# Optimization experiments

Measured on AMD Instinct MI355X. Metric: run time of the kernel, lower is better.

The kernel has to match this reference:

```python
import jax, jax.numpy as jnp
import numpy as np

B, H, I, E = 65536, 1024, 1024, 16

def setup_inputs() -> dict:
    key = jax.random.key(0)
    k1, k2, k3 = jax.random.split(key, 3)
    x = jax.random.normal(k1, (B, H), dtype=jnp.float32)
    Wg = jax.random.normal(k2, (E, H), dtype=jnp.float32) * 0.02   # gate weight [E, H]
    We = jax.random.normal(k3, (E, I, H), dtype=jnp.float32) * 0.02  # stacked expert weights [E, I, H]
    return {"x": x, "Wg": Wg, "We": We}

def reference(x, Wg, We):
    # gate scores and top-1 routing
    scores = x @ Wg.T                       # [B, E]
    expert_idx = jnp.argmax(scores, axis=-1)  # [B]
    onehot = jax.nn.one_hot(expert_idx, We.shape[0], dtype=x.dtype)  # [B, E]
    # each token goes through exactly one expert; sum of masked-input GEMMs
    out = jnp.zeros((x.shape[0], We.shape[1]), dtype=x.dtype)
    for e in range(We.shape[0]):  # fixed small expert count
        out = out + (x * onehot[:, e:e + 1]) @ We[e].T
    return out
```

## Files before the change

kernel.cpp:

```cpp
#include <hip/hip_runtime.h>
#include <hip/hip_bf16.h>

#define B_TOK 65536
#define HDIM  1024
#define EXP   16
#define IDIM  1024

typedef __attribute__((ext_vector_type(8))) short bf16x8_t;
typedef __attribute__((ext_vector_type(4))) float f32x4_t;


__device__ __forceinline__ unsigned short f2bf(float f) {
    unsigned int u = __float_as_uint(f);
    unsigned int r = (u + 0x7FFFu + ((u >> 16) & 1u)) >> 16;
    return (unsigned short)r;
}

__device__ __forceinline__ void async_load16(const void* g, void* l) {
    __builtin_amdgcn_global_load_lds(
        (const __attribute__((address_space(1))) unsigned int*)g,
        (__attribute__((address_space(3))) unsigned int*)l,
        16, 0, 0);
}

__global__ __launch_bounds__(256) void gate_kernel(
    const float* __restrict__ x, const float* __restrict__ Wg,
    unsigned short* __restrict__ xbf, int* __restrict__ eidx,
    int* __restrict__ cnts)
{
    __shared__ float wg[EXP * HDIM];
    const int tid = threadIdx.x;
    if (blockIdx.x == 0 && tid < EXP) cnts[tid] = 0;
    {
        const f32x4_t* s = (const f32x4_t*)Wg;
        f32x4_t* d = (f32x4_t*)wg;
        for (int i = tid; i < EXP * HDIM / 4; i += 256) d[i] = s[i];
    }
    __syncthreads();

    const int wid = tid >> 6, lane = tid & 63;
    const int gw = blockIdx.x * 4 + wid;

    for (int it = 0; it < 4; ++it) {
        const int t0 = gw * 16 + it * 4;
        f32x4_t xv[4][4];
        float acc[4][EXP];
        #pragma unroll
        for (int t = 0; t < 4; ++t) {
            const f32x4_t* row = (const f32x4_t*)(x + (size_t)(t0 + t) * HDIM);
            #pragma unroll
            for (int j = 0; j < 4; ++j)
                xv[t][j] = __builtin_nontemporal_load(row + j * 64 + lane);
        }
        #pragma unroll
        for (int t = 0; t < 4; ++t)
            #pragma unroll
            for (int e = 0; e < EXP; ++e) acc[t][e] = 0.f;

        #pragma unroll
        for (int j = 0; j < 4; ++j) {
            #pragma unroll
            for (int e = 0; e < EXP; ++e) {
                f32x4_t wv = *(const f32x4_t*)(wg + e * HDIM + j * 256 + lane * 4);
                #pragma unroll
                for (int t = 0; t < 4; ++t) {
                    acc[t][e] += xv[t][j][0] * wv[0] + xv[t][j][1] * wv[1]
                               + xv[t][j][2] * wv[2] + xv[t][j][3] * wv[3];
                }
            }
        }
        #pragma unroll
        for (int t = 0; t < 4; ++t) {
            unsigned short* orow = xbf + (size_t)(t0 + t) * HDIM;
            #pragma unroll
            for (int j = 0; j < 4; ++j) {
                ushort4 o;
                o.x = f2bf(xv[t][j][0]); o.y = f2bf(xv[t][j][1]);
                o.z = f2bf(xv[t][j][2]); o.w = f2bf(xv[t][j][3]);
                *(ushort4*)(orow + j * 256 + lane * 4) = o;
            }
        }
        #pragma unroll
        for (int t = 0; t < 4; ++t) {
            #pragma unroll
            for (int d = 32; d >= 1; d >>= 1) {
                #pragma unroll
                for (int e = 0; e < EXP; ++e)
                    acc[t][e] += __shfl_xor(acc[t][e], d, 64);
            }
            int best = 0; float bv = acc[t][0];
            #pragma unroll
            for (int e = 1; e < EXP; ++e)
                if (acc[t][e] > bv) { bv = acc[t][e]; best = e; }
            if (lane == 0) eidx[t0 + t] = best;
        }
    }
}

__global__ __launch_bounds__(256) void convert_we(
    const float* __restrict__ we, unsigned short* __restrict__ webf)
{
    const size_t n4 = (size_t)EXP * IDIM * HDIM / 4;
    const size_t stride = (size_t)gridDim.x * 256;
    for (size_t i = (size_t)blockIdx.x * 256 + threadIdx.x; i < n4; i += stride) {
        f32x4_t v = __builtin_nontemporal_load((const f32x4_t*)we + i);
        ushort4 o;
        o.x = f2bf(v[0]); o.y = f2bf(v[1]); o.z = f2bf(v[2]); o.w = f2bf(v[3]);
        ((ushort4*)webf)[i] = o;
    }
}

__global__ __launch_bounds__(256) void scatter_kernel(
    const int* __restrict__ eidx, int* __restrict__ token_list,
    int* __restrict__ counts)
{
    const int b = blockIdx.x * 256 + threadIdx.x;
    const int lane = threadIdx.x & 63;
    const int e = eidx[b];
    unsigned long long mymask = 0;
    int baseval = 0;
    #pragma unroll
    for (int ex = 0; ex < EXP; ++ex) {
        unsigned long long m = __ballot(e == ex);
        if (e == ex) mymask = m;
        int c = __popcll(m);
        if (lane == ex && c) baseval = atomicAdd(&counts[ex], c);
    }
    const int base = __shfl(baseval, e, 64);
    const int pos = base + __popcll(mymask & ((1ull << lane) - 1ull));
    token_list[(size_t)e * B_TOK + pos] = b;
}

__global__ __launch_bounds__(256) void moe_gemm(
    const unsigned short* __restrict__ xbf,
    const unsigned short* __restrict__ webf,
    const int* __restrict__ token_list,
    const int* __restrict__ counts,
    float* __restrict__ out)
{
    const int lin = blockIdx.x + 512 * (blockIdx.y + 8 * blockIdx.z);
    const int logical = (lin & 7) * 8192 + (lin >> 3);
    const int mt = logical & 511;
    const int nt = (logical >> 9) & 7;
    const int e  = logical >> 12;

    const int cnt = counts[e];
    const int m0 = mt * 128;
    if (m0 >= cnt) return;
    const int row_count = min(128, cnt - m0);
    const int n0 = nt * 128;

    __shared__ unsigned short As0[128 * 64];
    __shared__ unsigned short Bs0[128 * 64];
    __shared__ unsigned short As1[128 * 64];
    __shared__ unsigned short Bs1[128 * 64];

    const int tid = threadIdx.x;
    const int wid = tid >> 6, lane = tid & 63;
    const int rgrp = tid >> 3;
    const int kseg = tid & 7;
    const int ksw  = kseg ^ (rgrp & 7);

    const int* tl = token_list + (size_t)e * B_TOK + m0;
    size_t abase[4], bbase[4];
    #pragma unroll
    for (int i = 0; i < 4; ++i) {
        const int r = i * 32 + rgrp;
        const int tok = tl[min(r, row_count - 1)];
        abase[i] = ((size_t)tok * HDIM + ksw * 8) * 2;
        bbase[i] = (((size_t)e * IDIM + n0 + r) * HDIM + ksw * 8) * 2;
    }
    const char* xg = (const char*)xbf;
    const char* wp = (const char*)webf;

    f32x4_t acc[4][4];
    const f32x4_t z = {0.f, 0.f, 0.f, 0.f};
    #pragma unroll
    for (int mi = 0; mi < 4; ++mi)
        #pragma unroll
        for (int ni = 0; ni < 4; ++ni) acc[mi][ni] = z;

    const int wm = wid >> 1, wn = wid & 1;
    const int quad = lane >> 4, l16 = lane & 15;
    const int rx = l16 & 7;
    const int s0 = (quad ^ rx) << 3;
    const int s1 = ((quad + 4) ^ rx) << 3;
    const int arow0 = (wm * 64 + l16) * 64;
    const int brow0 = (wn * 64 + l16) * 64;

#define STAGE(AP, BP, K0)                                                      \
    { _Pragma("unroll")                                                        \
      for (int i = 0; i < 4; ++i) {                                            \
        async_load16(xg + abase[i] + (size_t)(K0) * 2,                         \
                     (char*)(AP) + i * 4096 + tid * 16);                       \
        async_load16(wp + bbase[i] + (size_t)(K0) * 2,                         \
                     (char*)(BP) + i * 4096 + tid * 16);                       \
      } }

#define COMPUTE(AP, BP)                                                        \
    { _Pragma("unroll")                                                        \
      for (int kkh = 0; kkh < 2; ++kkh) {                                      \
        const int co = kkh ? s1 : s0;                                          \
        bf16x8_t av[4], bv[4];                                                 \
        _Pragma("unroll")                                                      \
        for (int mi = 0; mi < 4; ++mi)                                         \
            av[mi] = *(const bf16x8_t*)((AP) + arow0 + mi * 1024 + co);        \
        _Pragma("unroll")                                                      \
        for (int ni = 0; ni < 4; ++ni)                                         \
            bv[ni] = *(const bf16x8_t*)((BP) + brow0 + ni * 1024 + co);        \
        _Pragma("unroll")                                                      \
        for (int mi = 0; mi < 4; ++mi)                                         \
            _Pragma("unroll")                                                  \
            for (int ni = 0; ni < 4; ++ni)                                     \
                acc[mi][ni] = __builtin_amdgcn_mfma_f32_16x16x32_bf16(         \
                    av[mi], bv[ni], acc[mi][ni], 0, 0, 0);                     \
      } }

    STAGE(As0, Bs0, 0);
    __syncthreads();

    for (int t = 0; t < 16; t += 2) {
        STAGE(As1, Bs1, (t + 1) * 64);
        COMPUTE(As0, Bs0);
        __syncthreads();
        if (t + 2 < 16) STAGE(As0, Bs0, (t + 2) * 64);
        COMPUTE(As1, Bs1);
        __syncthreads();
    }

    #pragma unroll
    for (int mi = 0; mi < 4; ++mi) {
        const int rl0 = wm * 64 + mi * 16 + quad * 4;
        #pragma unroll
        for (int r = 0; r < 4; ++r) {
            const int rl = rl0 + r;
            if (rl < row_count) {
                const int tok = tl[rl];
                float* orow = out + (size_t)tok * IDIM + n0 + wn * 64 + l16;
                #pragma unroll
                for (int ni = 0; ni < 4; ++ni)
                    __builtin_nontemporal_store(acc[mi][ni][r], orow + ni * 16);
            }
        }
    }
#undef STAGE
#undef COMPUTE
}

extern "C" void kernel_launch(void* const* d_in, const int* in_sizes, int n_in,
                              void* d_out, int out_size, void* d_ws, size_t ws_size,
                              hipStream_t stream) {
    const float* x  = (const float*)d_in[0];
    const float* Wg = (const float*)d_in[1];
    const float* We = (const float*)d_in[2];
    float* out = (float*)d_out;

    char* ws = (char*)d_ws;
    unsigned short* xbf   = (unsigned short*)(ws);
    unsigned short* webf  = (unsigned short*)(ws + 134217728);
    int*            eidx  = (int*)(ws + 167772160);
    int*            cnts  = (int*)(ws + 168034304);
    int*            tlist = (int*)(ws + 168034560);

    gate_kernel<<<1024, 256, 0, stream>>>(x, Wg, xbf, eidx, cnts);
    convert_we<<<4096, 256, 0, stream>>>(We, webf);
    scatter_kernel<<<256, 256, 0, stream>>>(eidx, tlist, cnts);
    moe_gemm<<<dim3(512, 8, 16), 256, 0, stream>>>(xbf, webf, tlist, cnts, out);
}
```

Baseline: 970.9 us.

## Fuse prep kernels and retile MoE GEMM to 128x256 with triple-buffered pipeline

Merges gate scoring, weight bf16 conversion and token scattering into one prep kernel. Extra blocks convert the weights, and each token is appended to its expert list with a per-token atomic instead of a separate ballot-based scatter pass. The grouped GEMM moves to 512-thread blocks with 128x256 output tiles and a three-stage LDS ring using explicit vmcnt waits, raw barriers and setprio, so more loads stay in flight and barrier stalls shrink. In exchange it caps per-expert tiles at 48 (6144 tokens) and uses about 144KB of LDS per block, which limits occupancy to one block per CU.

```diff
diff --git a/kernel.cpp b/kernel.cpp
--- a/kernel.cpp
+++ b/kernel.cpp
@@ -23,14 +23,27 @@
         16, 0, 0);
 }
 
-__global__ __launch_bounds__(256) void gate_kernel(
+__global__ __launch_bounds__(256) void prep_kernel(
     const float* __restrict__ x, const float* __restrict__ Wg,
-    unsigned short* __restrict__ xbf, int* __restrict__ eidx,
-    int* __restrict__ cnts)
+    const float* __restrict__ we,
+    unsigned short* __restrict__ xbf, unsigned short* __restrict__ webf,
+    int* __restrict__ token_list, int* __restrict__ cnts)
 {
+    const int tid = threadIdx.x;
+
+    if (blockIdx.x >= 1024) {
+        const size_t n4 = (size_t)EXP * IDIM * HDIM / 4;
+        const size_t stride = (size_t)512 * 256;
+        for (size_t i = (size_t)(blockIdx.x - 1024) * 256 + tid; i < n4; i += stride) {
+            f32x4_t v = __builtin_nontemporal_load((const f32x4_t*)we + i);
+            ushort4 o;
+            o.x = f2bf(v[0]); o.y = f2bf(v[1]); o.z = f2bf(v[2]); o.w = f2bf(v[3]);
+            ((ushort4*)webf)[i] = o;
+        }
+        return;
+    }
+
     __shared__ float wg[EXP * HDIM];
-    const int tid = threadIdx.x;
-    if (blockIdx.x == 0 && tid < EXP) cnts[tid] = 0;
     {
         const f32x4_t* s = (const f32x4_t*)Wg;
         f32x4_t* d = (f32x4_t*)wg;
@@ -92,83 +105,52 @@
             #pragma unroll
             for (int e = 1; e < EXP; ++e)
                 if (acc[t][e] > bv) { bv = acc[t][e]; best = e; }
-            if (lane == 0) eidx[t0 + t] = best;
-        }
-    }
-}
-
-__global__ __launch_bounds__(256) void convert_we(
-    const float* __restrict__ we, unsigned short* __restrict__ webf)
-{
-    const size_t n4 = (size_t)EXP * IDIM * HDIM / 4;
-    const size_t stride = (size_t)gridDim.x * 256;
-    for (size_t i = (size_t)blockIdx.x * 256 + threadIdx.x; i < n4; i += stride) {
-        f32x4_t v = __builtin_nontemporal_load((const f32x4_t*)we + i);
-        ushort4 o;
-        o.x = f2bf(v[0]); o.y = f2bf(v[1]); o.z = f2bf(v[2]); o.w = f2bf(v[3]);
-        ((ushort4*)webf)[i] = o;
-    }
-}
-
-__global__ __launch_bounds__(256) void scatter_kernel(
-    const int* __restrict__ eidx, int* __restrict__ token_list,
-    int* __restrict__ counts)
-{
-    const int b = blockIdx.x * 256 + threadIdx.x;
-    const int lane = threadIdx.x & 63;
-    const int e = eidx[b];
-    unsigned long long mymask = 0;
-    int baseval = 0;
-    #pragma unroll
-    for (int ex = 0; ex < EXP; ++ex) {
-        unsigned long long m = __ballot(e == ex);
-        if (e == ex) mymask = m;
-        int c = __popcll(m);
-        if (lane == ex && c) baseval = atomicAdd(&counts[ex], c);
-    }
-    const int base = __shfl(baseval, e, 64);
-    const int pos = base + __popcll(mymask & ((1ull << lane) - 1ull));
-    token_list[(size_t)e * B_TOK + pos] = b;
-}
-
-__global__ __launch_bounds__(256) void moe_gemm(
+            if (lane == 0) {
+                const int pos = atomicAdd(&cnts[best], 1);
+                token_list[(size_t)best * B_TOK + pos] = t0 + t;
+            }
+        }
+    }
+}
+
+__global__ __launch_bounds__(512, 2) void moe_gemm(
     const unsigned short* __restrict__ xbf,
     const unsigned short* __restrict__ webf,
     const int* __restrict__ token_list,
     const int* __restrict__ counts,
     float* __restrict__ out)
 {
-    const int lin = blockIdx.x + 512 * (blockIdx.y + 8 * blockIdx.z);
-    const int logical = (lin & 7) * 8192 + (lin >> 3);
-    const int mt = logical & 511;
-    const int nt = (logical >> 9) & 7;
-    const int e  = logical >> 12;
+    const int lin = blockIdx.x + 4 * (blockIdx.y + 48 * (int)blockIdx.z);
+    const int logical = (lin & 7) * 384 + (lin >> 3);
+    const int mt = logical % 48;
+    const int nt = (logical / 48) & 3;
+    const int e  = logical / 192;
 
     const int cnt = counts[e];
     const int m0 = mt * 128;
     if (m0 >= cnt) return;
     const int row_count = min(128, cnt - m0);
-    const int n0 = nt * 128;
-
-    __shared__ unsigned short As0[128 * 64];
-    __shared__ unsigned short Bs0[128 * 64];
-    __shared__ unsigned short As1[128 * 64];
-    __shared__ unsigned short Bs1[128 * 64];
+    const int n0 = nt * 256;
+
+    __shared__ unsigned short lds[3 * 24576];
 
     const int tid = threadIdx.x;
     const int wid = tid >> 6, lane = tid & 63;
-    const int rgrp = tid >> 3;
-    const int kseg = tid & 7;
-    const int ksw  = kseg ^ (rgrp & 7);
+    const int lrow = lane >> 3;
+    const int ksw  = (lane & 7) ^ lrow;
 
     const int* tl = token_list + (size_t)e * B_TOK + m0;
-    size_t abase[4], bbase[4];
-    #pragma unroll
-    for (int i = 0; i < 4; ++i) {
-        const int r = i * 32 + rgrp;
+    size_t abase[2], bbase[4];
+    #pragma unroll
+    for (int j = 0; j < 2; ++j) {
+        const int r = j * 64 + wid * 8 + lrow;
         const int tok = tl[min(r, row_count - 1)];
-        abase[i] = ((size_t)tok * HDIM + ksw * 8) * 2;
-        bbase[i] = (((size_t)e * IDIM + n0 + r) * HDIM + ksw * 8) * 2;
+        abase[j] = ((size_t)tok * HDIM + ksw * 8) * 2;
+    }
+    #pragma unroll
+    for (int j = 0; j < 4; ++j) {
+        const int r = j * 64 + wid * 8 + lrow;
+        bbase[j] = (((size_t)e * IDIM + n0 + r) * HDIM + ksw * 8) * 2;
     }
     const char* xg = (const char*)xbf;
     const char* wp = (const char*)webf;
@@ -180,7 +162,7 @@
         #pragma unroll
         for (int ni = 0; ni < 4; ++ni) acc[mi][ni] = z;
 
-    const int wm = wid >> 1, wn = wid & 1;
+    const int wm = wid >> 2, wn = wid & 3;
     const int quad = lane >> 4, l16 = lane & 15;
     const int rx = l16 & 7;
     const int s0 = (quad ^ rx) << 3;
@@ -188,26 +170,31 @@
     const int arow0 = (wm * 64 + l16) * 64;
     const int brow0 = (wn * 64 + l16) * 64;
 
-#define STAGE(AP, BP, K0)                                                      \
+#define LDSA(S) (lds + (S) * 24576)
+#define LDSB(S) (lds + (S) * 24576 + 8192)
+
+#define STAGE(S, T)                                                            \
     { _Pragma("unroll")                                                        \
-      for (int i = 0; i < 4; ++i) {                                            \
-        async_load16(xg + abase[i] + (size_t)(K0) * 2,                         \
-                     (char*)(AP) + i * 4096 + tid * 16);                       \
-        async_load16(wp + bbase[i] + (size_t)(K0) * 2,                         \
-                     (char*)(BP) + i * 4096 + tid * 16);                       \
-      } }
-
-#define COMPUTE(AP, BP)                                                        \
+      for (int j = 0; j < 2; ++j)                                              \
+        async_load16(xg + abase[j] + (size_t)(T) * 128,                        \
+                     (char*)LDSA(S) + (j * 512 + wid * 64 + lane) * 16);       \
+      _Pragma("unroll")                                                        \
+      for (int j = 0; j < 4; ++j)                                              \
+        async_load16(wp + bbase[j] + (size_t)(T) * 128,                        \
+                     (char*)LDSB(S) + (j * 512 + wid * 64 + lane) * 16);       \
+    }
+
+#define COMPUTE(S)                                                             \
     { _Pragma("unroll")                                                        \
       for (int kkh = 0; kkh < 2; ++kkh) {                                      \
         const int co = kkh ? s1 : s0;                                          \
         bf16x8_t av[4], bv[4];                                                 \
         _Pragma("unroll")                                                      \
         for (int mi = 0; mi < 4; ++mi)                                         \
-            av[mi] = *(const bf16x8_t*)((AP) + arow0 + mi * 1024 + co);        \
+            av[mi] = *(const bf16x8_t*)(LDSA(S) + arow0 + mi * 1024 + co);     \
         _Pragma("unroll")                                                      \
         for (int ni = 0; ni < 4; ++ni)                                         \
-            bv[ni] = *(const bf16x8_t*)((BP) + brow0 + ni * 1024 + co);        \
+            bv[ni] = *(const bf16x8_t*)(LDSB(S) + brow0 + ni * 1024 + co);     \
         _Pragma("unroll")                                                      \
         for (int mi = 0; mi < 4; ++mi)                                         \
             _Pragma("unroll")                                                  \
@@ -216,16 +203,31 @@
                     av[mi], bv[ni], acc[mi][ni], 0, 0, 0);                     \
       } }
 
-    STAGE(As0, Bs0, 0);
-    __syncthreads();
-
-    for (int t = 0; t < 16; t += 2) {
-        STAGE(As1, Bs1, (t + 1) * 64);
-        COMPUTE(As0, Bs0);
-        __syncthreads();
-        if (t + 2 < 16) STAGE(As0, Bs0, (t + 2) * 64);
-        COMPUTE(As1, Bs1);
-        __syncthreads();
+    STAGE(0, 0)
+    STAGE(1, 1)
+    asm volatile("s_waitcnt vmcnt(6)" ::: "memory");
+    __builtin_amdgcn_s_barrier();
+    __builtin_amdgcn_sched_barrier(0);
+
+    #pragma unroll
+    for (int t = 0; t < 16; ++t) {
+        const int s = t % 3;
+        if (t + 2 < 16) {
+            const int s2 = (t + 2) % 3;
+            STAGE(s2, t + 2)
+        }
+        __builtin_amdgcn_s_setprio(1);
+        COMPUTE(s)
+        __builtin_amdgcn_s_setprio(0);
+        if (t + 2 < 16) {
+            asm volatile("s_waitcnt vmcnt(6)" ::: "memory");
+        } else if (t + 1 < 16) {
+            asm volatile("s_waitcnt vmcnt(0)" ::: "memory");
+        }
+        if (t + 1 < 16) {
+            __builtin_amdgcn_s_barrier();
+            __builtin_amdgcn_sched_barrier(0);
+        }
     }
 
     #pragma unroll
@@ -245,6 +247,8 @@
     }
 #undef STAGE
 #undef COMPUTE
+#undef LDSA
+#undef LDSB
 }
 
 extern "C" void kernel_launch(void* const* d_in, const int* in_sizes, int n_in,
@@ -258,12 +262,10 @@
     char* ws = (char*)d_ws;
     unsigned short* xbf   = (unsigned short*)(ws);
     unsigned short* webf  = (unsigned short*)(ws + 134217728);
-    int*            eidx  = (int*)(ws + 167772160);
-    int*            cnts  = (int*)(ws + 168034304);
-    int*            tlist = (int*)(ws + 168034560);
-
-    gate_kernel<<<1024, 256, 0, stream>>>(x, Wg, xbf, eidx, cnts);
-    convert_we<<<4096, 256, 0, stream>>>(We, webf);
-    scatter_kernel<<<256, 256, 0, stream>>>(eidx, tlist, cnts);
-    moe_gemm<<<dim3(512, 8, 16), 256, 0, stream>>>(xbf, webf, tlist, cnts, out);
-}
+    int*            tlist = (int*)(ws + 167772160);
+    int*            cnts  = (int*)(ws + 171966464);
+
+    hipMemsetAsync(cnts, 0, EXP * sizeof(int), stream);
+    prep_kernel<<<1536, 256, 0, stream>>>(x, Wg, We, xbf, webf, tlist, cnts);
+    moe_gemm<<<dim3(4, 48, 16), 512, 0, stream>>>(xbf, webf, tlist, cnts, out);
+}
```

Measured after the change: 1.329 ms. +36.8%, slower.
